# Optimization experiments

Measured on AMD Instinct MI355X. Metric: run time of the kernel, lower is better.

The kernel has to match this reference:

```python
import jax, jax.numpy as jnp
import numpy as np

N, E, IN, HID, H, C, L, G = 20000, 640000, 128, 256, 8, 32, 5, 64
NEG_SLOPE = 0.2


def _layernorm(x, g, b, eps=1e-5):
    mu = jnp.mean(x, axis=-1, keepdims=True)
    var = jnp.mean((x - mu) ** 2, axis=-1, keepdims=True)
    return (x - mu) * jax.lax.rsqrt(var + eps) * g + b


def _gatv2(h, src, dst, Wl, bl, Wr, br, att, out_bias):
    # h: [N, HID]; src/dst: [E+N] (self loops appended)
    n = h.shape[0]
    xl = (h @ Wl + bl).reshape(n, H, C)  # source transform
    xr = (h @ Wr + br).reshape(n, H, C)  # target transform
    e = jax.nn.leaky_relu(xl[src] + xr[dst], NEG_SLOPE)       # [Etot, H, C]
    logits = jnp.einsum('ehc,hc->eh', e, att)                  # [Etot, H]
    m = jax.ops.segment_max(logits, dst, num_segments=n)       # segment softmax over dst
    a = jnp.exp(logits - m[dst])
    s = jax.ops.segment_sum(a, dst, num_segments=n)
    alpha = a / (s[dst] + 1e-16)                               # [Etot, H]
    out = jax.ops.segment_sum(alpha[:, :, None] * xl[src], dst, num_segments=n)
    return out.reshape(n, HID) + out_bias


def setup_inputs() -> dict:
    key = jax.random.key(0)
    ks = jax.random.split(key, 16)
    sc = 0.05
    inp = {
        'x': jax.random.normal(ks[0], (N, IN), jnp.float32),
        'edge_index': jax.random.randint(ks[1], (2, E), 0, N, jnp.int64),
        'batch': jnp.sort(jax.random.randint(ks[2], (N,), 0, G, jnp.int64)),
        'proj_W': jax.random.normal(ks[3], (IN, HID), jnp.float32) * sc,
        'proj_b': jnp.zeros((HID,), jnp.float32),
        'Wl': jax.random.normal(ks[4], (L, HID, HID), jnp.float32) * sc,
        'bl': jnp.zeros((L, HID), jnp.float32),
        'Wr': jax.random.normal(ks[5], (L, HID, HID), jnp.float32) * sc,
        'br': jnp.zeros((L, HID), jnp.float32),
        'att': jax.random.normal(ks[6], (L, H, C), jnp.float32) * sc,
        'out_bias': jnp.zeros((L, HID), jnp.float32),
        'ln_g': jnp.ones((L, HID), jnp.float32),
        'ln_b': jnp.zeros((L, HID), jnp.float32),
    }
    return inp


def reference(x, edge_index, batch, proj_W, proj_b, Wl, bl, Wr, br, att, out_bias, ln_g, ln_b):
    n = x.shape[0]
    loops = jnp.arange(n, dtype=edge_index.dtype)
    src = jnp.concatenate([edge_index[0], loops])  # add_self_loops=True
    dst = jnp.concatenate([edge_index[1], loops])
    h = x @ proj_W + proj_b
    for i in range(L):  # dropout = identity in eval mode
        conv = _gatv2(h, src, dst, Wl[i], bl[i], Wr[i], br[i], att[i], out_bias[i])
        h = _layernorm(h + jax.nn.elu(conv), ln_g[i], ln_b[i])
    counts = jax.ops.segment_sum(jnp.ones((n,), h.dtype), batch, num_segments=G)
    gsum = jax.ops.segment_sum(h, batch, num_segments=G)
    graph_emb = gsum / jnp.maximum(counts, 1.0)[:, None]  # global_mean_pool
    return graph_emb, h, batch
```

## Files before the change

### kernel.cpp

```cpp
#include <hip/hip_runtime.h>
#include <hip/hip_bf16.h>

#define NN   20000
#define NE   640000
#define INF_ 128
#define HID  256
#define NL   5
#define NG   64


typedef __hip_bfloat16 bf16;
typedef __attribute__((ext_vector_type(4))) float f32x4;
typedef __attribute__((ext_vector_type(8))) short bf16x8;

#if __has_builtin(__builtin_amdgcn_exp2f)
#define EXP2F __builtin_amdgcn_exp2f
#else
#define EXP2F exp2f
#endif

__device__ __forceinline__ float b2f(bf16 v) { return __bfloat162float(v); }
__device__ __forceinline__ short f2bs(float v) {
  union { bf16 h; short s; } u; u.h = __float2bfloat16(v); return u.s;
}
__device__ __forceinline__ f32x4 ldbf4(const bf16* p) {
  const ushort4 u = *(const ushort4*)p;
  union { unsigned short s; bf16 h; } c;
  f32x4 r;
  c.s = u.x; r[0] = b2f(c.h);
  c.s = u.y; r[1] = b2f(c.h);
  c.s = u.z; r[2] = b2f(c.h);
  c.s = u.w; r[3] = b2f(c.h);
  return r;
}
__device__ __forceinline__ f32x4 ldbf4o(const char* __restrict__ basep, unsigned off) {
  const uint2 u = *(const uint2*)(basep + off);
  f32x4 r;
  r[0] = __uint_as_float(u.x << 16);
  r[1] = __uint_as_float(u.x & 0xffff0000u);
  r[2] = __uint_as_float(u.y << 16);
  r[3] = __uint_as_float(u.y & 0xffff0000u);
  return r;
}

__global__ void detect_kernel(const int* __restrict__ ei,
                              const int* __restrict__ batch,
                              int* __restrict__ flags) {
  if (blockIdx.x == 0 && threadIdx.x == 0) {
    int e64 = 1, b64 = 1;
    for (int k = 0; k < 40; ++k) {
      if (ei[2 * (k * 15999) + 1] != 0) e64 = 0;
      if (batch[2 * (k * 249) + 1] != 0) b64 = 0;
    }
    flags[0] = e64;
    flags[1] = b64;
  }
}

__device__ __forceinline__ int ld_i(const int* p, int f, size_t idx) {
  return f ? p[2 * idx] : p[idx];
}

__global__ void hist_kernel(const int* __restrict__ ei, const int* __restrict__ flags,
                            int* __restrict__ deg) {
  int e = blockIdx.x * blockDim.x + threadIdx.x;
  if (e >= NE) return;
  int f = flags[0];
  int d = ld_i(ei, f, (size_t)NE + e);
  if ((unsigned)d < NN) atomicAdd(&deg[d], 1);
}

__global__ void scan_kernel(const int* __restrict__ deg, int* __restrict__ off,
                            int* __restrict__ tmp) {
  __shared__ int part[256];
  const int t = threadIdx.x;
  const int CH = (NN + 255) / 256;
  int b0 = t * CH;
  int b1 = b0 + CH; if (b1 > NN) b1 = NN; if (b0 > NN) b0 = NN;
  int s = 0;
  for (int i = b0; i < b1; ++i) s += deg[i];
  part[t] = s;
  __syncthreads();
  for (int d = 1; d < 256; d <<= 1) {
    int v = (t >= d) ? part[t - d] : 0;
    __syncthreads();
    part[t] += v;
    __syncthreads();
  }
  int pre = (t == 0) ? 0 : part[t - 1];
  for (int i = b0; i < b1; ++i) {
    off[i] = pre; tmp[i] = pre; pre += deg[i];
  }
  if (t == 0) off[NN] = part[255];
}

__global__ void scatter_kernel(const int* __restrict__ ei, const int* __restrict__ flags,
                               int* __restrict__ tmp, int* __restrict__ csr) {
  int e = blockIdx.x * blockDim.x + threadIdx.x;
  if (e >= NE) return;
  int f = flags[0];
  int d = ld_i(ei, f, (size_t)NE + e);
  int s = ld_i(ei, f, (size_t)e);
  if ((unsigned)d < NN) {
    int p = atomicAdd(&tmp[d], 1);
    int sv = ((unsigned)s < NN) ? s : 0;
    if ((unsigned)p < NE) csr[p] = sv * (HID * 2);
  }
}

template<int K, bool A_BF16>
__global__ __launch_bounds__(256) void gemm_bias_kernel(
    const void* __restrict__ Av, const float* __restrict__ B,
    const float* __restrict__ bias, float* __restrict__ Cf,
    bf16* __restrict__ Cb, int M)
{
  constexpr int N = 256;
  constexpr int LDB = K + 8;
  __shared__ __align__(16) short bT[32 * LDB];
  const int tid = threadIdx.x;
  const int n0 = blockIdx.x * 32;
  const int m_base = blockIdx.y * 256;

  if (tid < K) {
    const float* brow = B + (size_t)tid * N + n0;
#pragma unroll
    for (int j = 0; j < 32; ++j) bT[j * LDB + tid] = f2bs(brow[j]);
  }
  __syncthreads();

  const int wave = tid >> 6;
  const int lane = tid & 63;
  const int r    = lane & 15;
  const int quad = lane >> 4;
  const int m_wave = m_base + wave * 64;

  f32x4 acc[4][2];
#pragma unroll
  for (int i = 0; i < 4; ++i) { acc[i][0] = (f32x4)0.0f; acc[i][1] = (f32x4)0.0f; }

#pragma unroll
  for (int kk = 0; kk < K / 32; ++kk) {
    const int kof = kk * 32 + quad * 8;
    bf16x8 b0 = *(const bf16x8*)&bT[r * LDB + kof];
    bf16x8 b1 = *(const bf16x8*)&bT[(r + 16) * LDB + kof];
#pragma unroll
    for (int sm = 0; sm < 4; ++sm) {
      const int row = m_wave + sm * 16 + r;
      bf16x8 a = (bf16x8)(short)0;
      if (row < M) {
        if constexpr (A_BF16) {
          a = *(const bf16x8*)((const short*)Av + (size_t)row * K + kof);
        } else {
          const float* ap = (const float*)Av + (size_t)row * K + kof;
          f32x4 lo = *(const f32x4*)ap;
          f32x4 hi = *(const f32x4*)(ap + 4);
#pragma unroll
          for (int j = 0; j < 4; ++j) { a[j] = f2bs(lo[j]); a[4 + j] = f2bs(hi[j]); }
        }
      }
      acc[sm][0] = __builtin_amdgcn_mfma_f32_16x16x32_bf16(a, b0, acc[sm][0], 0, 0, 0);
      acc[sm][1] = __builtin_amdgcn_mfma_f32_16x16x32_bf16(a, b1, acc[sm][1], 0, 0, 0);
    }
  }

  const float bv0 = bias[n0 + r];
  const float bv1 = bias[n0 + 16 + r];
#pragma unroll
  for (int sm = 0; sm < 4; ++sm) {
#pragma unroll
    for (int rg = 0; rg < 4; ++rg) {
      const int row = m_wave + sm * 16 + quad * 4 + rg;
      if (row < M) {
        size_t i0 = (size_t)row * N + n0 + r;
        float v0 = acc[sm][0][rg] + bv0;
        float v1 = acc[sm][1][rg] + bv1;
        if (Cf) { Cf[i0] = v0; Cf[i0 + 16] = v1; }
        if (Cb) {
          ((unsigned short*)Cb)[i0]      = (unsigned short)f2bs(v0);
          ((unsigned short*)Cb)[i0 + 16] = (unsigned short)f2bs(v1);
        }
      }
    }
  }
}

template<bool A_BF16>
__global__ __launch_bounds__(256) void gemm_dual_kernel(
    const void* __restrict__ Av,
    const float* __restrict__ Bl, const float* __restrict__ Br,
    const float* __restrict__ bl, const float* __restrict__ br,
    bf16* __restrict__ Cl, bf16* __restrict__ Cr, int M)
{
  constexpr int K = HID, N = 256;
  constexpr int LDB = K + 8;
  __shared__ __align__(16) short bTl[32 * LDB];
  __shared__ __align__(16) short bTr[32 * LDB];
  const int tid = threadIdx.x;
  const int n0 = blockIdx.x * 32;
  const int m_base = blockIdx.y * 256;

  {
    const float* browl = Bl + (size_t)tid * N + n0;
    const float* browr = Br + (size_t)tid * N + n0;
#pragma unroll
    for (int j = 0; j < 32; ++j) {
      bTl[j * LDB + tid] = f2bs(browl[j]);
      bTr[j * LDB + tid] = f2bs(browr[j]);
    }
  }
  __syncthreads();

  const int wave = tid >> 6;
  const int lane = tid & 63;
  const int r    = lane & 15;
  const int quad = lane >> 4;
  const int m_wave = m_base + wave * 64;

  f32x4 accl[4][2], accr[4][2];
#pragma unroll
  for (int i = 0; i < 4; ++i) {
    accl[i][0] = (f32x4)0.0f; accl[i][1] = (f32x4)0.0f;
    accr[i][0] = (f32x4)0.0f; accr[i][1] = (f32x4)0.0f;
  }

#pragma unroll
  for (int kk = 0; kk < K / 32; ++kk) {
    const int kof = kk * 32 + quad * 8;
    bf16x8 b0l = *(const bf16x8*)&bTl[r * LDB + kof];
    bf16x8 b1l = *(const bf16x8*)&bTl[(r + 16) * LDB + kof];
    bf16x8 b0r = *(const bf16x8*)&bTr[r * LDB + kof];
    bf16x8 b1r = *(const bf16x8*)&bTr[(r + 16) * LDB + kof];
#pragma unroll
    for (int sm = 0; sm < 4; ++sm) {
      const int row = m_wave + sm * 16 + r;
      bf16x8 a = (bf16x8)(short)0;
      if (row < M) {
        if constexpr (A_BF16) {
          a = *(const bf16x8*)((const short*)Av + (size_t)row * K + kof);
        } else {
          const float* ap = (const float*)Av + (size_t)row * K + kof;
          f32x4 lo = *(const f32x4*)ap;
          f32x4 hi = *(const f32x4*)(ap + 4);
#pragma unroll
          for (int j = 0; j < 4; ++j) { a[j] = f2bs(lo[j]); a[4 + j] = f2bs(hi[j]); }
        }
      }
      accl[sm][0] = __builtin_amdgcn_mfma_f32_16x16x32_bf16(a, b0l, accl[sm][0], 0, 0, 0);
      accl[sm][1] = __builtin_amdgcn_mfma_f32_16x16x32_bf16(a, b1l, accl[sm][1], 0, 0, 0);
      accr[sm][0] = __builtin_amdgcn_mfma_f32_16x16x32_bf16(a, b0r, accr[sm][0], 0, 0, 0);
      accr[sm][1] = __builtin_amdgcn_mfma_f32_16x16x32_bf16(a, b1r, accr[sm][1], 0, 0, 0);
    }
  }

  const float bl0v = bl[n0 + r],  bl1v = bl[n0 + 16 + r];
  const float br0v = br[n0 + r],  br1v = br[n0 + 16 + r];
#pragma unroll
  for (int sm = 0; sm < 4; ++sm) {
#pragma unroll
    for (int rg = 0; rg < 4; ++rg) {
      const int row = m_wave + sm * 16 + quad * 4 + rg;
      if (row < M) {
        size_t i0 = (size_t)row * N + n0 + r;
        ((unsigned short*)Cl)[i0]      = (unsigned short)f2bs(accl[sm][0][rg] + bl0v);
        ((unsigned short*)Cl)[i0 + 16] = (unsigned short)f2bs(accl[sm][1][rg] + bl1v);
        ((unsigned short*)Cr)[i0]      = (unsigned short)f2bs(accr[sm][0][rg] + br0v);
        ((unsigned short*)Cr)[i0 + 16] = (unsigned short)f2bs(accr[sm][1][rg] + br1v);
      }
    }
  }
}

__device__ __forceinline__ float hsum8(float v) {
  v += __shfl_xor(v, 1);  v += __shfl_xor(v, 2);  v += __shfl_xor(v, 4);
  return v;
}
__device__ __forceinline__ float wsum64(float v) {
  v += __shfl_xor(v, 1);  v += __shfl_xor(v, 2);  v += __shfl_xor(v, 4);
  v += __shfl_xor(v, 8);  v += __shfl_xor(v, 16); v += __shfl_xor(v, 32);
  return v;
}

__global__ __launch_bounds__(256) void gat_layer_kernel(
    const bf16* __restrict__ xl, const bf16* __restrict__ xr,
    float* __restrict__ h, bf16* __restrict__ h_bf,
    const int* __restrict__ off, const int* __restrict__ csr,
    const float* __restrict__ att, const float* __restrict__ outb,
    const float* __restrict__ lng, const float* __restrict__ lnb)
{
  const int lane = threadIdx.x & 63;
  const int node = blockIdx.x * 4 + (threadIdx.x >> 6);
  const int cb   = ((lane >> 3) << 5) + ((lane & 7) << 2);
  const unsigned cb2  = (unsigned)cb * 2;
  const unsigned selfo = (unsigned)node * (HID * 2) + cb2;
  const size_t base = (size_t)node * HID + cb;
  const char* xlc = (const char*)xl;

  const f32x4 xrv = ldbf4o((const char*)xr, selfo);
  const f32x4 xls = ldbf4o(xlc, selfo);
  f32x4 avs = *(const f32x4*)(att + cb);
#pragma unroll
  for (int c = 0; c < 4; ++c) avs[c] *= 1.44269504f;

  float pa = 0.f;
#pragma unroll
  for (int c = 0; c < 4; ++c) {
    float z = xls[c] + xrv[c];
    float e = fmaxf(z, 0.2f * z);
    pa = fmaf(avs[c], e, pa);
  }
  const float es = EXP2F(hsum8(pa));
  float s = es;
  f32x4 o;
#pragma unroll
  for (int c = 0; c < 4; ++c) o[c] = es * xls[c];

  int beg = off[node], end = off[node + 1];
  if (beg < 0) beg = 0;
  if (end > NE) end = NE;
  const unsigned* csrb = (const unsigned*)csr;

  int p = beg;
  for (; p + 4 <= end; p += 4) {
    const unsigned o0 = csrb[p]     + cb2;
    const unsigned o1 = csrb[p + 1] + cb2;
    const unsigned o2 = csrb[p + 2] + cb2;
    const unsigned o3 = csrb[p + 3] + cb2;
    const f32x4 x0 = ldbf4o(xlc, o0);
    const f32x4 x1 = ldbf4o(xlc, o1);
    const f32x4 x2 = ldbf4o(xlc, o2);
    const f32x4 x3 = ldbf4o(xlc, o3);
    float p0 = 0.f, p1 = 0.f, p2 = 0.f, p3 = 0.f;
#pragma unroll
    for (int c = 0; c < 4; ++c) {
      float z0 = x0[c] + xrv[c]; z0 = fmaxf(z0, 0.2f * z0);
      float z1 = x1[c] + xrv[c]; z1 = fmaxf(z1, 0.2f * z1);
      float z2 = x2[c] + xrv[c]; z2 = fmaxf(z2, 0.2f * z2);
      float z3 = x3[c] + xrv[c]; z3 = fmaxf(z3, 0.2f * z3);
      p0 = fmaf(avs[c], z0, p0);
      p1 = fmaf(avs[c], z1, p1);
      p2 = fmaf(avs[c], z2, p2);
      p3 = fmaf(avs[c], z3, p3);
    }
    const float e0 = EXP2F(hsum8(p0));
    const float e1 = EXP2F(hsum8(p1));
    const float e2 = EXP2F(hsum8(p2));
    const float e3 = EXP2F(hsum8(p3));
    s += (e0 + e1) + (e2 + e3);
#pragma unroll
    for (int c = 0; c < 4; ++c)
      o[c] = fmaf(e0, x0[c], fmaf(e1, x1[c], fmaf(e2, x2[c], fmaf(e3, x3[c], o[c]))));
  }
  for (; p < end; ++p) {
    const unsigned oo = csrb[p] + cb2;
    const f32x4 xv = ldbf4o(xlc, oo);
    float pe = 0.f;
#pragma unroll
    for (int c = 0; c < 4; ++c) {
      float z = xv[c] + xrv[c];
      float e = fmaxf(z, 0.2f * z);
      pe = fmaf(avs[c], e, pe);
    }
    const float ee = EXP2F(hsum8(pe));
    s += ee;
#pragma unroll
    for (int c = 0; c < 4; ++c) o[c] = fmaf(ee, xv[c], o[c]);
  }

  const f32x4 ob  = *(const f32x4*)(outb + cb);
  const f32x4 hv  = *(const f32x4*)(h + base);
  const float inv_s = 1.f / s;
  f32x4 res;
#pragma unroll
  for (int c = 0; c < 4; ++c) {
    float conv = fmaf(o[c], inv_s, ob[c]);
    float el = conv > 0.f ? conv : (__expf(conv) - 1.f);
    res[c] = hv[c] + el;
  }
  float pr = (res[0] + res[1]) + (res[2] + res[3]);
  const float mu = wsum64(pr) * (1.f / 256.f);
  f32x4 dv;
  float p2s = 0.f;
#pragma unroll
  for (int c = 0; c < 4; ++c) { dv[c] = res[c] - mu; p2s = fmaf(dv[c], dv[c], p2s); }
  const float var = wsum64(p2s) * (1.f / 256.f);
  const float rs = rsqrtf(var + 1e-5f);
  const f32x4 g4 = *(const f32x4*)(lng + cb);
  const f32x4 b4 = *(const f32x4*)(lnb + cb);
  f32x4 y;
#pragma unroll
  for (int c = 0; c < 4; ++c) y[c] = fmaf(dv[c] * rs, g4[c], b4[c]);

  *(f32x4*)(h + base) = y;
  if (h_bf) {
    ushort4 u;
    u.x = (unsigned short)f2bs(y[0]);
    u.y = (unsigned short)f2bs(y[1]);
    u.z = (unsigned short)f2bs(y[2]);
    u.w = (unsigned short)f2bs(y[3]);
    *(ushort4*)((unsigned short*)h_bf + base) = u;
  }
}

__global__ __launch_bounds__(256) void pool_kernel(
    const float* __restrict__ h, const int* __restrict__ batch,
    const int* __restrict__ flags, float* __restrict__ gsum, int* __restrict__ gcnt)
{
  const int t = threadIdx.x;
  const int f = flags[1];
  int n0 = blockIdx.x * 80;
  int n1 = n0 + 80; if (n1 > NN) n1 = NN;
  float acc = 0.f;
  int g_cur = ld_i(batch, f, n0);
  if ((unsigned)g_cur >= NG) g_cur = 0;
  int run = 0;
  for (int n = n0; n < n1; ++n) {
    int g = ld_i(batch, f, n);
    if ((unsigned)g >= NG) g = 0;
    if (g != g_cur) {
      atomicAdd(&gsum[(size_t)g_cur * HID + t], acc);
      if (t == 0) atomicAdd(&gcnt[g_cur], run);
      acc = 0.f; run = 0; g_cur = g;
    }
    acc += h[(size_t)n * HID + t];
    ++run;
  }
  atomicAdd(&gsum[(size_t)g_cur * HID + t], acc);
  if (t == 0) atomicAdd(&gcnt[g_cur], run);
}

__global__ void write_out_kernel(const float* __restrict__ gsum, const int* __restrict__ gcnt,
                                 const int* __restrict__ batch,
                                 const int* __restrict__ flags, float* __restrict__ out)
{
  int i = blockIdx.x * blockDim.x + threadIdx.x;
  if (i < NG * HID) {
    int g = i >> 8;
    float c = (float)gcnt[g];
    c = c > 1.f ? c : 1.f;
    out[i] = gsum[i] / c;
  } else if (i < NG * HID + NN) {
    int n = i - NG * HID;
    int f = flags[1];
    out[(size_t)NG * HID + (size_t)NN * HID + n] = (float)ld_i(batch, f, (size_t)n);
  }
}

extern "C" void kernel_launch(void* const* d_in, const int* in_sizes, int n_in,
                              void* d_out, int out_size, void* d_ws, size_t ws_size,
                              hipStream_t stream) {
  (void)in_sizes; (void)n_in; (void)out_size;

  const float* x     = (const float*)d_in[0];
  const int*   ei    = (const int*)d_in[1];
  const int*   batch = (const int*)d_in[2];
  const float* projW = (const float*)d_in[3];
  const float* projB = (const float*)d_in[4];
  const float* Wl    = (const float*)d_in[5];
  const float* bl    = (const float*)d_in[6];
  const float* Wr    = (const float*)d_in[7];
  const float* br    = (const float*)d_in[8];
  const float* att   = (const float*)d_in[9];
  const float* outb  = (const float*)d_in[10];
  const float* lng   = (const float*)d_in[11];
  const float* lnb   = (const float*)d_in[12];
  float* out = (float*)d_out;

  float* h = out + (size_t)NG * HID;

  char* ws = (char*)d_ws;
  size_t o = 0;
  auto alloc = [&](size_t bytes) -> void* {
    void* p = ws + o;
    o += (bytes + 255) & ~(size_t)255;
    return p;
  };
  int*   flags = (int*)alloc(4 * 4);
  int*   deg   = (int*)alloc((size_t)NN * 4);
  int*   offs  = (int*)alloc((size_t)(NN + 1) * 4);
  int*   tmp   = (int*)alloc((size_t)NN * 4);
  float* gsum  = (float*)alloc((size_t)NG * HID * 4);
  int*   gcnt  = (int*)alloc((size_t)NG * 4);
  int*   csr   = (int*)alloc((size_t)NE * 4);
  bf16*  xl    = (bf16*)alloc((size_t)NN * HID * 2);
  bf16*  xr    = (bf16*)alloc((size_t)NN * HID * 2);
  size_t o_base = o;
  bf16*  h_bf  = (bf16*)alloc((size_t)NN * HID * 2);
  const bool use_hbf = (ws_size >= o);
  if (!use_hbf) { h_bf = nullptr; o = o_base; }

  hipMemsetAsync(deg, 0, (size_t)NN * 4, stream);
  hipMemsetAsync(gsum, 0, (size_t)NG * HID * 4 + (size_t)NG * 4, stream);

  detect_kernel<<<1, 64, 0, stream>>>(ei, batch, flags);

  hist_kernel<<<(NE + 255) / 256, 256, 0, stream>>>(ei, flags, deg);
  scan_kernel<<<1, 256, 0, stream>>>(deg, offs, tmp);
  scatter_kernel<<<(NE + 255) / 256, 256, 0, stream>>>(ei, flags, tmp, csr);

  dim3 gg(HID / 32, (NN + 255) / 256);

  gemm_bias_kernel<INF_, false><<<gg, 256, 0, stream>>>(x, projW, projB, h, h_bf, NN);

  for (int i = 0; i < NL; ++i) {
    if (use_hbf) {
      gemm_dual_kernel<true><<<gg, 256, 0, stream>>>(h_bf,
          Wl + (size_t)i * HID * HID, Wr + (size_t)i * HID * HID,
          bl + (size_t)i * HID, br + (size_t)i * HID, xl, xr, NN);
    } else {
      gemm_dual_kernel<false><<<gg, 256, 0, stream>>>(h,
          Wl + (size_t)i * HID * HID, Wr + (size_t)i * HID * HID,
          bl + (size_t)i * HID, br + (size_t)i * HID, xl, xr, NN);
    }
    gat_layer_kernel<<<NN / 4, 256, 0, stream>>>(xl, xr, h, h_bf, offs, csr,
                                                 att + (size_t)i * HID, outb + (size_t)i * HID,
                                                 lng + (size_t)i * HID, lnb + (size_t)i * HID);
  }

  pool_kernel<<<250, 256, 0, stream>>>(h, batch, flags, gsum, gcnt);
  write_out_kernel<<<(NG * HID + NN + 255) / 256, 256, 0, stream>>>(gsum, gcnt, batch, flags, out);
}
```

Baseline: 625.7 us.

## Use DPP reductions, abs-based leaky ReLU, scalar offsets, and 8-wide edge unroll

```diff
diff --git a/kernel.cpp b/kernel.cpp
--- a/kernel.cpp
+++ b/kernel.cpp
@@ -42,6 +42,37 @@
   r[3] = __uint_as_float(u.y & 0xffff0000u);
   return r;
 }
+
+#if __has_builtin(__builtin_amdgcn_update_dpp)
+template<int CTRL>
+__device__ __forceinline__ float dpp_add(float v) {
+  int t = __builtin_amdgcn_update_dpp(0, __float_as_int(v), CTRL, 0xF, 0xF, true);
+  return v + __int_as_float(t);
+}
+__device__ __forceinline__ float hsum8(float v) {
+  v = dpp_add<0xB1>(v);
+  v = dpp_add<0x4E>(v);
+  v = dpp_add<0x141>(v);
+  return v;
+}
+__device__ __forceinline__ float wsum64(float v) {
+  v = hsum8(v);
+  v = dpp_add<0x140>(v);
+  v += __shfl_xor(v, 16);
+  v += __shfl_xor(v, 32);
+  return v;
+}
+#else
+__device__ __forceinline__ float hsum8(float v) {
+  v += __shfl_xor(v, 1);  v += __shfl_xor(v, 2);  v += __shfl_xor(v, 4);
+  return v;
+}
+__device__ __forceinline__ float wsum64(float v) {
+  v += __shfl_xor(v, 1);  v += __shfl_xor(v, 2);  v += __shfl_xor(v, 4);
+  v += __shfl_xor(v, 8);  v += __shfl_xor(v, 16); v += __shfl_xor(v, 32);
+  return v;
+}
+#endif
 
 __global__ void detect_kernel(const int* __restrict__ ei,
                               const int* __restrict__ batch,
@@ -270,16 +301,6 @@
   }
 }
 
-__device__ __forceinline__ float hsum8(float v) {
-  v += __shfl_xor(v, 1);  v += __shfl_xor(v, 2);  v += __shfl_xor(v, 4);
-  return v;
-}
-__device__ __forceinline__ float wsum64(float v) {
-  v += __shfl_xor(v, 1);  v += __shfl_xor(v, 2);  v += __shfl_xor(v, 4);
-  v += __shfl_xor(v, 8);  v += __shfl_xor(v, 16); v += __shfl_xor(v, 32);
-  return v;
-}
-
 __global__ __launch_bounds__(256) void gat_layer_kernel(
     const bf16* __restrict__ xl, const bf16* __restrict__ xr,
     float* __restrict__ h, bf16* __restrict__ h_bf,
@@ -288,7 +309,7 @@
     const float* __restrict__ lng, const float* __restrict__ lnb)
 {
   const int lane = threadIdx.x & 63;
-  const int node = blockIdx.x * 4 + (threadIdx.x >> 6);
+  const int node = __builtin_amdgcn_readfirstlane(blockIdx.x * 4 + (threadIdx.x >> 6));
   const int cb   = ((lane >> 3) << 5) + ((lane & 7) << 2);
   const unsigned cb2  = (unsigned)cb * 2;
   const unsigned selfo = (unsigned)node * (HID * 2) + cb2;
@@ -297,16 +318,20 @@
 
   const f32x4 xrv = ldbf4o((const char*)xr, selfo);
   const f32x4 xls = ldbf4o(xlc, selfo);
-  f32x4 avs = *(const f32x4*)(att + cb);
-#pragma unroll
-  for (int c = 0; c < 4; ++c) avs[c] *= 1.44269504f;
+  const f32x4 av = *(const f32x4*)(att + cb);
+  f32x4 a6, a4;
+#pragma unroll
+  for (int c = 0; c < 4; ++c) {
+    a6[c] = av[c] * (0.6f * 1.44269504f);
+    a4[c] = av[c] * (0.4f * 1.44269504f);
+  }
 
   float pa = 0.f;
 #pragma unroll
   for (int c = 0; c < 4; ++c) {
     float z = xls[c] + xrv[c];
-    float e = fmaxf(z, 0.2f * z);
-    pa = fmaf(avs[c], e, pa);
+    pa = fmaf(a6[c], z, pa);
+    pa = fmaf(a4[c], fabsf(z), pa);
   }
   const float es = EXP2F(hsum8(pa));
   float s = es;
@@ -314,41 +339,41 @@
 #pragma unroll
   for (int c = 0; c < 4; ++c) o[c] = es * xls[c];
 
-  int beg = off[node], end = off[node + 1];
+  int beg = __builtin_amdgcn_readfirstlane(off[node]);
+  int end = __builtin_amdgcn_readfirstlane(off[node + 1]);
   if (beg < 0) beg = 0;
   if (end > NE) end = NE;
   const unsigned* csrb = (const unsigned*)csr;
 
   int p = beg;
-  for (; p + 4 <= end; p += 4) {
-    const unsigned o0 = csrb[p]     + cb2;
-    const unsigned o1 = csrb[p + 1] + cb2;
-    const unsigned o2 = csrb[p + 2] + cb2;
-    const unsigned o3 = csrb[p + 3] + cb2;
-    const f32x4 x0 = ldbf4o(xlc, o0);
-    const f32x4 x1 = ldbf4o(xlc, o1);
-    const f32x4 x2 = ldbf4o(xlc, o2);
-    const f32x4 x3 = ldbf4o(xlc, o3);
-    float p0 = 0.f, p1 = 0.f, p2 = 0.f, p3 = 0.f;
+  for (; p + 8 <= end; p += 8) {
+    unsigned ofs[8];
+#pragma unroll
+    for (int j = 0; j < 8; ++j) ofs[j] = csrb[p + j] + cb2;
+    f32x4 xv[8];
+#pragma unroll
+    for (int j = 0; j < 8; ++j) xv[j] = ldbf4o(xlc, ofs[j]);
+    float e[8];
+#pragma unroll
+    for (int j = 0; j < 8; ++j) {
+      float acc = 0.f;
+#pragma unroll
+      for (int c = 0; c < 4; ++c) {
+        float z = xv[j][c] + xrv[c];
+        acc = fmaf(a6[c], z, acc);
+        acc = fmaf(a4[c], fabsf(z), acc);
+      }
+      e[j] = EXP2F(hsum8(acc));
+    }
+    s += (((e[0] + e[1]) + (e[2] + e[3])) + ((e[4] + e[5]) + (e[6] + e[7])));
 #pragma unroll
     for (int c = 0; c < 4; ++c) {
-      float z0 = x0[c] + xrv[c]; z0 = fmaxf(z0, 0.2f * z0);
-      float z1 = x1[c] + xrv[c]; z1 = fmaxf(z1, 0.2f * z1);
-      float z2 = x2[c] + xrv[c]; z2 = fmaxf(z2, 0.2f * z2);
-      float z3 = x3[c] + xrv[c]; z3 = fmaxf(z3, 0.2f * z3);
-      p0 = fmaf(avs[c], z0, p0);
-      p1 = fmaf(avs[c], z1, p1);
-      p2 = fmaf(avs[c], z2, p2);
-      p3 = fmaf(avs[c], z3, p3);
-    }
-    const float e0 = EXP2F(hsum8(p0));
-    const float e1 = EXP2F(hsum8(p1));
-    const float e2 = EXP2F(hsum8(p2));
-    const float e3 = EXP2F(hsum8(p3));
-    s += (e0 + e1) + (e2 + e3);
-#pragma unroll
-    for (int c = 0; c < 4; ++c)
-      o[c] = fmaf(e0, x0[c], fmaf(e1, x1[c], fmaf(e2, x2[c], fmaf(e3, x3[c], o[c]))));
+      float c0 = fmaf(e[0], xv[0][c], fmaf(e[1], xv[1][c],
+                 fmaf(e[2], xv[2][c], fmaf(e[3], xv[3][c], o[c]))));
+      float c1 = fmaf(e[4], xv[4][c], fmaf(e[5], xv[5][c],
+                 fmaf(e[6], xv[6][c], e[7] * xv[7][c])));
+      o[c] = c0 + c1;
+    }
   }
   for (; p < end; ++p) {
     const unsigned oo = csrb[p] + cb2;
@@ -357,8 +382,8 @@
 #pragma unroll
     for (int c = 0; c < 4; ++c) {
       float z = xv[c] + xrv[c];
-      float e = fmaxf(z, 0.2f * z);
-      pe = fmaf(avs[c], e, pe);
+      pe = fmaf(a6[c], z, pe);
+      pe = fmaf(a4[c], fabsf(z), pe);
     }
     const float ee = EXP2F(hsum8(pe));
     s += ee;
```

New measurement: 600.2 us. 1.04x faster.
